# Optimization experiments

Measured on AMD Instinct MI355X. Metric: run time of the kernel, lower is better.

## Reference

```python
import jax, jax.numpy as jnp
import numpy as np


def setup_inputs() -> dict:
    key = jax.random.key(0)
    ks = jax.random.split(key, 6)
    B, S, D, E = 4, 8192, 2048, 8
    scale = 1.0 / np.sqrt(D)
    return {
        "x": jax.random.normal(ks[0], (B, S, D), dtype=jnp.float32),
        "Wg": jax.random.normal(ks[1], (E, D), dtype=jnp.float32) * scale,
        "bg": jax.random.normal(ks[2], (E,), dtype=jnp.float32) * scale,
        "Wn": jax.random.normal(ks[3], (E, D), dtype=jnp.float32) * scale,
        "bn": jax.random.normal(ks[4], (E,), dtype=jnp.float32) * scale,
        "noise": jax.random.normal(ks[5], (B, S, E), dtype=jnp.float32),
        "k": 2,
    }


def reference(x, Wg, bg, Wn, bn, noise, k):
    # gate and noisy-gate projections: [B,S,D] x [E,D] -> [B,S,E]
    gate_logits = jnp.einsum("bsd,ed->bse", x, Wg) + bg
    noisy_pre = jnp.einsum("bsd,ed->bse", x, Wn) + bn
    noisy_logits = noise * jax.nn.softplus(noisy_pre) + gate_logits

    # top-k over experts (largest, sorted), matching torch.topk
    topklogits, topexperts = jax.lax.top_k(noisy_logits, k)  # [B,S,k]

    # softmax over sparse logits (-inf elsewhere) == softmax over the topk
    # values, scattered back; small E,k so a one-hot scatter is cheap.
    topk_probs = jax.nn.softmax(topklogits, axis=-1)          # [B,S,k]
    onehot = jax.nn.one_hot(topexperts, noisy_logits.shape[-1],
                            dtype=topk_probs.dtype)           # [B,S,k,E]
    router_output = jnp.einsum("bsk,bske->bse", topk_probs, onehot)
    return router_output, topexperts
```

## Files before the change

### kernel.cpp

```cpp
#include <hip/hip_runtime.h>
#include <math.h>


#define RD 2048
#define RE 8
#define NE16 16
#define TOKB 64
#define CH 32
#define NW 4

#define AS1 __attribute__((address_space(1)))
#define AS3 __attribute__((address_space(3)))

__device__ __forceinline__ void gload_lds16(const float* g, float* l) {
    __builtin_amdgcn_global_load_lds((const AS1 unsigned int*)g,
                                     (AS3 unsigned int*)l, 16, 0, 0);
}

__global__ __launch_bounds__(256) void transpose_w_kernel(
    const float* __restrict__ Wg, const float* __restrict__ Wn,
    float* __restrict__ WT)
{
    const int idx = blockIdx.x * 256 + threadIdx.x;
    const int d = idx >> 4;
    const int e = idx & 15;
    WT[idx] = (e < 8) ? Wg[e * RD + d] : Wn[(e - 8) * RD + d];
}

template <int KSL>
__global__ __launch_bounds__(256) void router_main_kernel(
    const float* __restrict__ x,
    const float* __restrict__ WT,
    float* __restrict__ pws,
    int T)
{
    constexpr int KLEN = RD / KSL;
    constexpr int NCH = KLEN / CH;
    __shared__ float xb[2][TOKB * CH];

    const int tid = threadIdx.x;
    const int w = tid >> 6;
    const int l = tid & 63;
    const int NTB = T / TOKB;
    const int bt = blockIdx.x % NTB;
    const int kslice = blockIdx.x / NTB;
    const int tokBase = bt * TOKB;
    const int kbase = kslice * KLEN;

    float acc[NE16];
#pragma unroll
    for (int e = 0; e < NE16; ++e) acc[e] = 0.f;

    {
#pragma unroll
        for (int s = 0; s < 2; ++s) {
            const int i = w * 2 + s;
            const int t = i * 8 + (l >> 3);
            const int p = l & 7;
            const float* gsrc = x + (size_t)(tokBase + t) * RD + kbase
                                + ((p ^ (t & 7)) << 2);
            gload_lds16(gsrc, &xb[0][i * 256]);
        }
    }
    __syncthreads();

#pragma unroll 1
    for (int c = 0; c < NCH; ++c) {
        const int buf = c & 1;

        if (c + 1 < NCH) {
#pragma unroll
            for (int s = 0; s < 2; ++s) {
                const int i = w * 2 + s;
                const int t = i * 8 + (l >> 3);
                const int p = l & 7;
                const float* gsrc = x + (size_t)(tokBase + t) * RD + kbase
                                    + (c + 1) * CH + ((p ^ (t & 7)) << 2);
                gload_lds16(gsrc, &xb[buf ^ 1][i * 256]);
            }
        }

        const int wbase = __builtin_amdgcn_readfirstlane(
            (kbase + c * CH + w * 8) * NE16);
        const float* __restrict__ wt = WT + wbase;
#pragma unroll
        for (int r = 0; r < 2; ++r) {
            const int q = w * 2 + r;
            const float4 xq = *reinterpret_cast<const float4*>(
                &xb[buf][l * CH + ((q ^ (l & 7)) << 2)]);
            const float xs[4] = {xq.x, xq.y, xq.z, xq.w};
#pragma unroll
            for (int ii = 0; ii < 4; ++ii) {
                const float* wrow = wt + (r * 4 + ii) * NE16;
#pragma unroll
                for (int e = 0; e < NE16; ++e)
                    acc[e] = fmaf(xs[ii], wrow[e], acc[e]);
            }
        }

        __syncthreads();
    }

    float* red = &xb[0][0];
    {
        const int roff = (w * TOKB + l) * NE16;
        *reinterpret_cast<float4*>(&red[roff + 0])  = make_float4(acc[0], acc[1], acc[2], acc[3]);
        *reinterpret_cast<float4*>(&red[roff + 4])  = make_float4(acc[4], acc[5], acc[6], acc[7]);
        *reinterpret_cast<float4*>(&red[roff + 8])  = make_float4(acc[8], acc[9], acc[10], acc[11]);
        *reinterpret_cast<float4*>(&red[roff + 12]) = make_float4(acc[12], acc[13], acc[14], acc[15]);
    }
    __syncthreads();

    {
        const int tok = tid >> 2;
        const int q4 = tid & 3;
        float4 s = make_float4(0.f, 0.f, 0.f, 0.f);
#pragma unroll
        for (int wv = 0; wv < NW; ++wv) {
            const float4 a = *reinterpret_cast<const float4*>(
                &red[(wv * TOKB + tok) * NE16 + q4 * 4]);
            s.x += a.x; s.y += a.y; s.z += a.z; s.w += a.w;
        }
        float* dst = pws + ((size_t)kslice * T + tokBase + tok) * NE16 + q4 * 4;
        *reinterpret_cast<float4*>(dst) = s;
    }
}

__global__ __launch_bounds__(256) void router_finalize_kernel(
    const float* __restrict__ pws,
    const float* __restrict__ bg,
    const float* __restrict__ bn,
    const float* __restrict__ noise,
    float* __restrict__ out_router,
    float* __restrict__ out_experts,
    int T, int ksl)
{
    const int tok = blockIdx.x * 256 + threadIdx.x;

    float g[RE], nn[RE];
#pragma unroll
    for (int e = 0; e < RE; ++e) { g[e] = bg[e]; nn[e] = bn[e]; }
#pragma unroll 1
    for (int s = 0; s < ksl; ++s) {
        const float* p = pws + ((size_t)s * T + tok) * NE16;
#pragma unroll
        for (int e = 0; e < RE; ++e) { g[e] += p[e]; nn[e] += p[8 + e]; }
    }

    const float4* nzp = reinterpret_cast<const float4*>(noise + (size_t)tok * RE);
    const float4 nz0 = nzp[0];
    const float4 nz1 = nzp[1];
    const float nzv[RE] = {nz0.x, nz0.y, nz0.z, nz0.w,
                           nz1.x, nz1.y, nz1.z, nz1.w};

    float v[RE];
#pragma unroll
    for (int e = 0; e < RE; ++e) {
        const float p = nn[e];
        const float sp = fmaxf(p, 0.f) + log1pf(expf(-fabsf(p)));
        v[e] = fmaf(nzv[e], sp, g[e]);
    }

    int i1 = 0; float m1 = v[0];
#pragma unroll
    for (int e = 1; e < RE; ++e)
        if (v[e] > m1) { m1 = v[e]; i1 = e; }
    int i2 = -1; float m2 = -INFINITY;
#pragma unroll
    for (int e = 0; e < RE; ++e)
        if (e != i1 && v[e] > m2) { m2 = v[e]; i2 = e; }

    const float e2 = expf(m2 - m1);
    const float inv = 1.f / (1.f + e2);
    const float p1s = inv;
    const float p2s = e2 * inv;

    float r[RE];
#pragma unroll
    for (int e = 0; e < RE; ++e)
        r[e] = (e == i1) ? p1s : ((e == i2) ? p2s : 0.f);

    float4* orow = reinterpret_cast<float4*>(out_router + (size_t)tok * RE);
    orow[0] = make_float4(r[0], r[1], r[2], r[3]);
    orow[1] = make_float4(r[4], r[5], r[6], r[7]);

    float2* erow = reinterpret_cast<float2*>(out_experts + (size_t)tok * 2);
    *erow = make_float2((float)i1, (float)i2);
}

extern "C" void kernel_launch(void* const* d_in, const int* in_sizes, int n_in,
                              void* d_out, int out_size, void* d_ws, size_t ws_size,
                              hipStream_t stream) {
    const float* x   = (const float*)d_in[0];
    const float* Wg  = (const float*)d_in[1];
    const float* bg  = (const float*)d_in[2];
    const float* Wn  = (const float*)d_in[3];
    const float* bn  = (const float*)d_in[4];
    const float* nz  = (const float*)d_in[5];
    const int T = in_sizes[0] / RD;

    float* WT  = (float*)d_ws;
    float* pws = WT + (size_t)RD * NE16;

    float* out_router  = (float*)d_out;
    float* out_experts = out_router + (size_t)T * RE;

    hipLaunchKernelGGL(transpose_w_kernel, dim3((RD * NE16) / 256), dim3(256),
                       0, stream, Wg, Wn, WT);

    const int NTB = T / TOKB;
    const size_t need4 = (size_t)RD * NE16 * 4 + (size_t)4 * T * NE16 * 4;
    if (ws_size >= need4) {
        hipLaunchKernelGGL(router_main_kernel<4>, dim3(NTB * 4), dim3(256), 0,
                           stream, x, WT, pws, T);
        hipLaunchKernelGGL(router_finalize_kernel, dim3(T / 256), dim3(256), 0,
                           stream, pws, bg, bn, nz, out_router, out_experts,
                           T, 4);
    } else {
        hipLaunchKernelGGL(router_main_kernel<2>, dim3(NTB * 2), dim3(256), 0,
                           stream, x, WT, pws, T);
        hipLaunchKernelGGL(router_finalize_kernel, dim3(T / 256), dim3(256), 0,
                           stream, pws, bg, bn, nz, out_router, out_experts,
                           T, 2);
    }
}
```

Before: 66.34 us.

## Deepen LDS prefetch to four buffers with vmcnt waits, fix k-split at two

Measured after the change: 60.77 us. -8.4%, faster.

```diff
diff --git a/kernel.cpp b/kernel.cpp
--- a/kernel.cpp
+++ b/kernel.cpp
@@ -7,10 +7,16 @@
 #define NE16 16
 #define TOKB 64
 #define CH 32
+#define KSL 2
+#define KLEN (RD / KSL)
+#define NCH (KLEN / CH)
 #define NW 4
+#define DEPTH 4
 
 #define AS1 __attribute__((address_space(1)))
 #define AS3 __attribute__((address_space(3)))
+
+#define WAITVM(N) asm volatile("s_waitcnt vmcnt(" #N ")" ::: "memory")
 
 __device__ __forceinline__ void gload_lds16(const float* g, float* l) {
     __builtin_amdgcn_global_load_lds((const AS1 unsigned int*)g,
@@ -27,16 +33,13 @@
     WT[idx] = (e < 8) ? Wg[e * RD + d] : Wn[(e - 8) * RD + d];
 }
 
-template <int KSL>
 __global__ __launch_bounds__(256) void router_main_kernel(
     const float* __restrict__ x,
     const float* __restrict__ WT,
     float* __restrict__ pws,
     int T)
 {
-    constexpr int KLEN = RD / KSL;
-    constexpr int NCH = KLEN / CH;
-    __shared__ float xb[2][TOKB * CH];
+    __shared__ float xb[DEPTH][TOKB * CH];
 
     const int tid = threadIdx.x;
     const int w = tid >> 6;
@@ -51,34 +54,33 @@
 #pragma unroll
     for (int e = 0; e < NE16; ++e) acc[e] = 0.f;
 
-    {
-#pragma unroll
-        for (int s = 0; s < 2; ++s) {
-            const int i = w * 2 + s;
-            const int t = i * 8 + (l >> 3);
-            const int p = l & 7;
-            const float* gsrc = x + (size_t)(tokBase + t) * RD + kbase
-                                + ((p ^ (t & 7)) << 2);
-            gload_lds16(gsrc, &xb[0][i * 256]);
-        }
-    }
-    __syncthreads();
+    const size_t laneoff = (size_t)(l >> 3) * RD + ((((l & 7) ^ (l >> 3))) << 2);
+    const float* p0 = x + (size_t)(tokBase + (w * 2 + 0) * 8) * RD + kbase + laneoff;
+    const float* p1 = x + (size_t)(tokBase + (w * 2 + 1) * 8) * RD + kbase + laneoff;
+    float* d0base = &xb[0][(w * 2 + 0) * 256];
+    float* d1base = &xb[0][(w * 2 + 1) * 256];
+
+    gload_lds16(p0 + 0 * CH, d0base + 0 * (TOKB * CH));
+    gload_lds16(p1 + 0 * CH, d1base + 0 * (TOKB * CH));
+    gload_lds16(p0 + 1 * CH, d0base + 1 * (TOKB * CH));
+    gload_lds16(p1 + 1 * CH, d1base + 1 * (TOKB * CH));
 
 #pragma unroll 1
     for (int c = 0; c < NCH; ++c) {
-        const int buf = c & 1;
-
-        if (c + 1 < NCH) {
-#pragma unroll
-            for (int s = 0; s < 2; ++s) {
-                const int i = w * 2 + s;
-                const int t = i * 8 + (l >> 3);
-                const int p = l & 7;
-                const float* gsrc = x + (size_t)(tokBase + t) * RD + kbase
-                                    + (c + 1) * CH + ((p ^ (t & 7)) << 2);
-                gload_lds16(gsrc, &xb[buf ^ 1][i * 256]);
-            }
+        const int b = c & (DEPTH - 1);
+
+        if (c + 2 < NCH) {
+            const int nb = (c + 2) & (DEPTH - 1);
+            gload_lds16(p0 + (c + 2) * CH, d0base + nb * (TOKB * CH));
+            gload_lds16(p1 + (c + 2) * CH, d1base + nb * (TOKB * CH));
+            WAITVM(4);
+        } else if (c + 2 == NCH) {
+            WAITVM(2);
+        } else {
+            WAITVM(0);
         }
+        __builtin_amdgcn_s_barrier();
+        __builtin_amdgcn_sched_barrier(0);
 
         const int wbase = __builtin_amdgcn_readfirstlane(
             (kbase + c * CH + w * 8) * NE16);
@@ -87,7 +89,7 @@
         for (int r = 0; r < 2; ++r) {
             const int q = w * 2 + r;
             const float4 xq = *reinterpret_cast<const float4*>(
-                &xb[buf][l * CH + ((q ^ (l & 7)) << 2)]);
+                &xb[b][l * CH + ((q ^ (l & 7)) << 2)]);
             const float xs[4] = {xq.x, xq.y, xq.z, xq.w};
 #pragma unroll
             for (int ii = 0; ii < 4; ++ii) {
@@ -97,9 +99,9 @@
                     acc[e] = fmaf(xs[ii], wrow[e], acc[e]);
             }
         }
-
-        __syncthreads();
-    }
+    }
+
+    __syncthreads();
 
     float* red = &xb[0][0];
     {
@@ -133,18 +135,18 @@
     const float* __restrict__ noise,
     float* __restrict__ out_router,
     float* __restrict__ out_experts,
-    int T, int ksl)
+    int T)
 {
     const int tok = blockIdx.x * 256 + threadIdx.x;
 
+    const float* pp0 = pws + (size_t)tok * NE16;
+    const float* pp1 = pws + ((size_t)T + tok) * NE16;
+
     float g[RE], nn[RE];
 #pragma unroll
-    for (int e = 0; e < RE; ++e) { g[e] = bg[e]; nn[e] = bn[e]; }
-#pragma unroll 1
-    for (int s = 0; s < ksl; ++s) {
-        const float* p = pws + ((size_t)s * T + tok) * NE16;
-#pragma unroll
-        for (int e = 0; e < RE; ++e) { g[e] += p[e]; nn[e] += p[8 + e]; }
+    for (int e = 0; e < RE; ++e) {
+        g[e]  = pp0[e] + pp1[e] + bg[e];
+        nn[e] = pp0[8 + e] + pp1[8 + e] + bn[e];
     }
 
     const float4* nzp = reinterpret_cast<const float4*>(noise + (size_t)tok * RE);
@@ -209,18 +211,9 @@
                        0, stream, Wg, Wn, WT);
 
     const int NTB = T / TOKB;
-    const size_t need4 = (size_t)RD * NE16 * 4 + (size_t)4 * T * NE16 * 4;
-    if (ws_size >= need4) {
-        hipLaunchKernelGGL(router_main_kernel<4>, dim3(NTB * 4), dim3(256), 0,
-                           stream, x, WT, pws, T);
-        hipLaunchKernelGGL(router_finalize_kernel, dim3(T / 256), dim3(256), 0,
-                           stream, pws, bg, bn, nz, out_router, out_experts,
-                           T, 4);
-    } else {
-        hipLaunchKernelGGL(router_main_kernel<2>, dim3(NTB * 2), dim3(256), 0,
-                           stream, x, WT, pws, T);
-        hipLaunchKernelGGL(router_finalize_kernel, dim3(T / 256), dim3(256), 0,
-                           stream, pws, bg, bn, nz, out_router, out_experts,
-                           T, 2);
-    }
-}
+    hipLaunchKernelGGL(router_main_kernel, dim3(NTB * KSL), dim3(256), 0,
+                       stream, x, WT, pws, T);
+
+    hipLaunchKernelGGL(router_finalize_kernel, dim3(T / 256), dim3(256), 0,
+                       stream, pws, bg, bn, nz, out_router, out_experts, T);
+}
```
